# Kernel tuning notes

Hardware: AMD Instinct MI355X
Metric: run time of the kernel (lower is better)

The kernel has to match this reference:

```python
import jax, jax.numpy as jnp
import numpy as np

B, T, INPUT_DIM = 4, 2048, 1024
N_HEADS, HEAD_DIM, EMB_DIM = 16, 64, 1024


def setup_inputs() -> dict:
    key = jax.random.key(0)
    ks = jax.random.split(key, 7)
    s = 0.02
    return {
        "k": jax.random.normal(ks[0], (B, T, INPUT_DIM), jnp.float32),
        "q": jax.random.normal(ks[1], (B, T, INPUT_DIM), jnp.float32),
        "v": jax.random.normal(ks[2], (B, T, INPUT_DIM), jnp.float32),
        # weights stored [in, out] (torch Linear applies x @ W.T with W [out,in])
        "w_key": jax.random.normal(ks[3], (INPUT_DIM, N_HEADS * HEAD_DIM), jnp.float32) * s,
        "w_query": jax.random.normal(ks[4], (INPUT_DIM, N_HEADS * HEAD_DIM), jnp.float32) * s,
        "w_value": jax.random.normal(ks[5], (INPUT_DIM, N_HEADS * HEAD_DIM), jnp.float32) * s,
        "w_proj": jax.random.normal(ks[6], (N_HEADS * HEAD_DIM, EMB_DIM), jnp.float32) * s,
    }


def reference(k, q, v, w_key, w_query, w_value, w_proj):
    temperature = np.sqrt(HEAD_DIM).astype(np.float32)
    # projections -> [B, T, H, D]
    kh = (k @ w_key).reshape(B, T, N_HEADS, HEAD_DIM)
    qh = (q @ w_query).reshape(B, T, N_HEADS, HEAD_DIM)
    vh = (v @ w_value).reshape(B, T, N_HEADS, HEAD_DIM)
    # scaled dot-product attention: scores [B, H, T, T]
    scores = jnp.einsum("bqhd,bkhd->bhqk", qh, kh) / temperature
    attn = jax.nn.softmax(scores, axis=-1)
    out = jnp.einsum("bhqk,bkhd->bqhd", attn, vh).reshape(B, T, N_HEADS * HEAD_DIM)
    return out @ w_proj
```

## Files before the change

### kernel.cpp

```cpp
#include <hip/hip_runtime.h>

typedef unsigned short bf16_t;
typedef __attribute__((ext_vector_type(8))) short short8;
typedef __attribute__((ext_vector_type(4))) float f32x4;
typedef __attribute__((ext_vector_type(16))) float f32x16;
typedef __attribute__((ext_vector_type(4))) unsigned short usx4;

#define T_SEQ 2048
#define NHEAD 16

__device__ __forceinline__ unsigned short f2bf(float x) {
  union { float f; unsigned u; } v; v.f = x;
  unsigned r = v.u + 0x7fffu + ((v.u >> 16) & 1u);
  return (unsigned short)(r >> 16);
}

__device__ __forceinline__ void gld_lds16(const void* g, void* l) {
  __builtin_amdgcn_global_load_lds((const __attribute__((address_space(1))) void*)g,
                                   (__attribute__((address_space(3))) void*)l, 16, 0, 0);
}

__global__ __launch_bounds__(256) void cvt_bf16(const float* __restrict__ in,
                                                bf16_t* __restrict__ out, int n4) {
  int i = blockIdx.x * 256 + threadIdx.x;
  const int stride = gridDim.x * 256;
  for (; i < n4; i += stride) {
    const float4 v = ((const float4*)in)[i];
    usx4 w = { f2bf(v.x), f2bf(v.y), f2bf(v.z), f2bf(v.w) };
    ((usx4*)out)[i] = w;
  }
}

__global__ __launch_bounds__(256) void wtrans(const float* __restrict__ w0, const float* __restrict__ w1,
                                              const float* __restrict__ w2, const float* __restrict__ w3,
                                              bf16_t* __restrict__ wt) {
  __shared__ float tile[32][33];
  const float* w = (blockIdx.z == 0) ? w0 : (blockIdx.z == 1) ? w1 : (blockIdx.z == 2) ? w2 : w3;
  bf16_t* o = wt + (size_t)blockIdx.z * 1024 * 1024;
  const int c = threadIdx.x & 31;
  const int r = threadIdx.x >> 5;
  const int k0 = blockIdx.y * 32, n0 = blockIdx.x * 32;
#pragma unroll
  for (int rr = 0; rr < 32; rr += 8)
    tile[r + rr][c] = w[(size_t)(k0 + r + rr) * 1024 + n0 + c];
  __syncthreads();
#pragma unroll
  for (int rr = 0; rr < 32; rr += 8)
    o[(size_t)(n0 + r + rr) * 1024 + k0 + c] = f2bf(tile[c][r + rr]);
}

template<int MODE>
__global__ __launch_bounds__(256) void gemm128(const bf16_t* __restrict__ A,
                                               const bf16_t* __restrict__ Bt,
                                               void* __restrict__ Cout, int K) {
  __shared__ bf16_t As[128 * 64];
  __shared__ bf16_t Bs[128 * 64];
  const int tid = threadIdx.x;
  const int lane = tid & 63;
  const int l15 = lane & 15;
  const int g = lane >> 4;
  const int wave = tid >> 6;
  const int wr = wave >> 1, wc = wave & 1;
  const int row0 = blockIdx.y * 128, col0 = blockIdx.x * 128;

  f32x4 acc[4][4];
#pragma unroll
  for (int m = 0; m < 4; ++m)
#pragma unroll
    for (int n = 0; n < 4; ++n) acc[m][n] = (f32x4){0.f, 0.f, 0.f, 0.f};

  const int r_st = tid >> 3;
  const int c_st = tid & 7;

  for (int kt = 0; kt < K; kt += 64) {
#pragma unroll
    for (int i = 0; i < 4; ++i) {
      const int r = r_st + i * 32;
      gld_lds16(A  + (size_t)(row0 + r) * K + kt + c_st * 8, As + (size_t)(tid + i * 256) * 8);
      gld_lds16(Bt + (size_t)(col0 + r) * K + kt + c_st * 8, Bs + (size_t)(tid + i * 256) * 8);
    }
    __syncthreads();
#pragma unroll
    for (int ks = 0; ks < 2; ++ks) {
      short8 a[4], b[4];
#pragma unroll
      for (int m = 0; m < 4; ++m)
        a[m] = *(const short8*)(As + (wr * 64 + m * 16 + l15) * 64 + ks * 32 + g * 8);
#pragma unroll
      for (int n = 0; n < 4; ++n)
        b[n] = *(const short8*)(Bs + (wc * 64 + n * 16 + l15) * 64 + ks * 32 + g * 8);
#pragma unroll
      for (int m = 0; m < 4; ++m)
#pragma unroll
        for (int n = 0; n < 4; ++n)
          acc[m][n] = __builtin_amdgcn_mfma_f32_16x16x32_bf16(a[m], b[n], acc[m][n], 0, 0, 0);
    }
    __syncthreads();
  }

  if constexpr (MODE == 0 || MODE == 1) {
    const float sc = (MODE == 1) ? 0.18033688011112042f : 1.0f;
    bf16_t* C = (bf16_t*)Cout;
#pragma unroll
    for (int m = 0; m < 4; ++m) {
      const int row = row0 + wr * 64 + m * 16 + g * 4;
#pragma unroll
      for (int n = 0; n < 4; ++n) {
        const int col = col0 + wc * 64 + n * 16 + l15;
#pragma unroll
        for (int i = 0; i < 4; ++i)
          C[(size_t)(row + i) * 1024 + col] = f2bf(acc[m][n][i] * sc);
      }
    }
  } else if constexpr (MODE == 2) {
    bf16_t* C = (bf16_t*)Cout;
#pragma unroll
    for (int m = 0; m < 4; ++m) {
      const int row = row0 + wr * 64 + m * 16 + g * 4;
      const int bb = row >> 11;
      const int t = row & 2047;
#pragma unroll
      for (int n = 0; n < 4; ++n) {
        const int col = col0 + wc * 64 + n * 16 + l15;
        const int hh = col >> 6, dd = col & 63;
        usx4 w = { f2bf(acc[m][n][0]), f2bf(acc[m][n][1]), f2bf(acc[m][n][2]), f2bf(acc[m][n][3]) };
        *(usx4*)(C + (((size_t)(bb * 16 + hh) * 64 + dd) * 2048 + t)) = w;
      }
    }
  } else {
    float* C = (float*)Cout;
#pragma unroll
    for (int m = 0; m < 4; ++m) {
      const int row = row0 + wr * 64 + m * 16 + g * 4;
#pragma unroll
      for (int n = 0; n < 4; ++n) {
        const int col = col0 + wc * 64 + n * 16 + l15;
#pragma unroll
        for (int i = 0; i < 4; ++i)
          C[(size_t)(row + i) * 1024 + col] = acc[m][n][i];
      }
    }
  }
}

__global__ __launch_bounds__(256) void attn_fwd(const bf16_t* __restrict__ qh,
                                                const bf16_t* __restrict__ kh,
                                                const bf16_t* __restrict__ vt,
                                                bf16_t* __restrict__ ao) {
  __shared__ bf16_t smem[8192];
  bf16_t* Ks = smem;
  bf16_t* Vs = smem + 4096;
  const int tid = threadIdx.x;
  const int lane = tid & 63;
  const int l31 = lane & 31;
  const int half = lane >> 5;
  const int wave = tid >> 6;
  const int qblk = blockIdx.x;
  const int bh = blockIdx.y;
  const int b = bh >> 4, h = bh & 15;

  const int tq = qblk * 128 + wave * 32 + l31;
  const size_t qoff = (size_t)(b * T_SEQ + tq) * 1024 + h * 64;
  short8 qf[4];
#pragma unroll
  for (int ks = 0; ks < 4; ++ks)
    qf[ks] = *(const short8*)(qh + qoff + ks * 16 + half * 8);

  f32x16 ov0, ov1;
#pragma unroll
  for (int i = 0; i < 16; ++i) { ov0[i] = 0.f; ov1[i] = 0.f; }
  float mrun = -1e30f, lrun = 0.f;

  const size_t kbase = (size_t)b * T_SEQ * 1024 + h * 64;
  const size_t vbase = (size_t)bh * 64 * T_SEQ;
  const int r_st = tid >> 3;
  const int cd = tid & 7;

  for (int kv = 0; kv < T_SEQ / 64; ++kv) {
    const int t0 = kv * 64;
#pragma unroll
    for (int i = 0; i < 2; ++i) {
      const int r = r_st + i * 32;
      const int cs = cd ^ (r & 7);
      gld_lds16(kh + kbase + (size_t)(t0 + r) * 1024 + cs * 8, Ks + (size_t)(tid + i * 256) * 8);
      gld_lds16(vt + vbase + (size_t)r * T_SEQ + t0 + cs * 8,  Vs + (size_t)(tid + i * 256) * 8);
    }
    __syncthreads();

    f32x16 st[2];
    __builtin_amdgcn_s_setprio(1);
#pragma unroll
    for (int t = 0; t < 2; ++t) {
#pragma unroll
      for (int i = 0; i < 16; ++i) st[t][i] = 0.f;
      const int row = t * 32 + l31;
#pragma unroll
      for (int ks = 0; ks < 4; ++ks) {
        const short8 af = *(const short8*)(Ks + row * 64 + (((ks * 2 + half) ^ (l31 & 7)) * 8));
        st[t] = __builtin_amdgcn_mfma_f32_32x32x16_bf16(af, qf[ks], st[t], 0, 0, 0);
      }
    }
    __builtin_amdgcn_s_setprio(0);

    float pm = st[0][0];
#pragma unroll
    for (int i = 1; i < 16; ++i) pm = fmaxf(pm, st[0][i]);
#pragma unroll
    for (int i = 0; i < 16; ++i) pm = fmaxf(pm, st[1][i]);
    pm = fmaxf(pm, __shfl_xor(pm, 32));

    if (__any(pm > mrun + 8.f)) {
      const float newm = fmaxf(mrun, pm);
      const float corr = __builtin_amdgcn_exp2f(mrun - newm);
      mrun = newm;
      lrun *= corr;
#pragma unroll
      for (int i = 0; i < 16; ++i) { ov0[i] *= corr; ov1[i] *= corr; }
    }

    float psum = 0.f;
#pragma unroll
    for (int t = 0; t < 2; ++t)
#pragma unroll
      for (int i = 0; i < 16; ++i) {
        const float p = __builtin_amdgcn_exp2f(st[t][i] - mrun);
        st[t][i] = p;
        psum += p;
      }
    psum += __shfl_xor(psum, 32);
    lrun += psum;

#pragma unroll
    for (int s = 0; s < 4; ++s) {
      const int t = s >> 1, base = (s & 1) * 8;
      unsigned c0, c1, c2, c3;
      asm("v_cvt_pk_bf16_f32 %0, %1, %2" : "=v"(c0) : "v"(st[t][base + 0]), "v"(st[t][base + 1]));
      asm("v_cvt_pk_bf16_f32 %0, %1, %2" : "=v"(c1) : "v"(st[t][base + 2]), "v"(st[t][base + 3]));
      asm("v_cvt_pk_bf16_f32 %0, %1, %2" : "=v"(c2) : "v"(st[t][base + 4]), "v"(st[t][base + 5]));
      asm("v_cvt_pk_bf16_f32 %0, %1, %2" : "=v"(c3) : "v"(st[t][base + 6]), "v"(st[t][base + 7]));
      asm("v_permlane32_swap_b32 %0, %1" : "+v"(c0), "+v"(c2));
      asm("v_permlane32_swap_b32 %0, %1" : "+v"(c1), "+v"(c3));
      union { short8 v; unsigned u[4]; } bu;
      bu.u[0] = c0; bu.u[1] = c1; bu.u[2] = c2; bu.u[3] = c3;
      __builtin_amdgcn_s_setprio(1);
#pragma unroll
      for (int dt = 0; dt < 2; ++dt) {
        const int row = dt * 32 + l31;
        const short8 av = *(const short8*)(Vs + row * 64 + (((s * 2 + half) ^ (l31 & 7)) * 8));
        if (dt == 0) ov0 = __builtin_amdgcn_mfma_f32_32x32x16_bf16(av, bu.v, ov0, 0, 0, 0);
        else         ov1 = __builtin_amdgcn_mfma_f32_32x32x16_bf16(av, bu.v, ov1, 0, 0, 0);
      }
      __builtin_amdgcn_s_setprio(0);
    }
    __syncthreads();
  }

  const float inv = 1.f / lrun;
  bf16_t* obuf = smem + wave * 2048;
#pragma unroll
  for (int k = 0; k < 4; ++k) {
    usx4 w0 = { f2bf(ov0[4 * k + 0] * inv), f2bf(ov0[4 * k + 1] * inv),
                f2bf(ov0[4 * k + 2] * inv), f2bf(ov0[4 * k + 3] * inv) };
    *(usx4*)(obuf + l31 * 64 + ((k ^ (l31 & 7)) * 8) + half * 4) = w0;
    usx4 w1 = { f2bf(ov1[4 * k + 0] * inv), f2bf(ov1[4 * k + 1] * inv),
                f2bf(ov1[4 * k + 2] * inv), f2bf(ov1[4 * k + 3] * inv) };
    *(usx4*)(obuf + l31 * 64 + (((4 + k) ^ (l31 & 7)) * 8) + half * 4) = w1;
  }
  __syncthreads();
  const int r = lane >> 1;
  const int cb = (lane & 1) * 4;
  const size_t orow = (size_t)(b * T_SEQ + qblk * 128 + wave * 32 + r) * 1024 + h * 64;
#pragma unroll
  for (int c = 0; c < 4; ++c) {
    const int ch = cb + c;
    const short8 v = *(const short8*)(obuf + r * 64 + ((ch ^ (r & 7)) * 8));
    *(short8*)(ao + orow + ch * 8) = v;
  }
}

extern "C" void kernel_launch(void* const* d_in, const int* in_sizes, int n_in,
                              void* d_out, int out_size, void* d_ws, size_t ws_size,
                              hipStream_t stream) {
  const float* k_in  = (const float*)d_in[0];
  const float* q_in  = (const float*)d_in[1];
  const float* v_in  = (const float*)d_in[2];
  const float* w_key = (const float*)d_in[3];
  const float* w_qry = (const float*)d_in[4];
  const float* w_val = (const float*)d_in[5];
  const float* w_prj = (const float*)d_in[6];

  char* ws = (char*)d_ws;
  bf16_t* xb = (bf16_t*)(ws);
  bf16_t* wt = (bf16_t*)(ws + (16u << 20));
  bf16_t* qh = (bf16_t*)(ws + (24u << 20));
  bf16_t* kh = (bf16_t*)(ws + (40u << 20));
  bf16_t* vt = (bf16_t*)(ws + (56u << 20));
  bf16_t* ao = (bf16_t*)(ws + (72u << 20));

  wtrans<<<dim3(32, 32, 4), 256, 0, stream>>>(w_key, w_qry, w_val, w_prj, wt);

  const int N4 = (8192 * 1024) / 4;
  cvt_bf16<<<2048, 256, 0, stream>>>(k_in, xb, N4);
  gemm128<0><<<dim3(8, 64), 256, 0, stream>>>(xb, wt + 0 * (1u << 20), kh, 1024);
  cvt_bf16<<<2048, 256, 0, stream>>>(q_in, xb, N4);
  gemm128<1><<<dim3(8, 64), 256, 0, stream>>>(xb, wt + 1 * (1u << 20), qh, 1024);
  cvt_bf16<<<2048, 256, 0, stream>>>(v_in, xb, N4);
  gemm128<2><<<dim3(8, 64), 256, 0, stream>>>(xb, wt + 2 * (1u << 20), vt, 1024);

  attn_fwd<<<dim3(16, 64), 256, 0, stream>>>(qh, kh, vt, ao);

  gemm128<3><<<dim3(8, 64), 256, 0, stream>>>(ao, wt + 3 * (1u << 20), d_out, 1024);
}
```

Before: 252.4 us.

## Fuse fp32-to-bf16 conversion into GEMM loads and double-buffer attention K/V tiles

Removes the three standalone cvt_bf16 passes by having the QKV projection GEMMs read fp32 activations directly and pack them to bf16 in registers before storing to LDS. The attention kernel now double-buffers its K/V tiles so the next tile's loads overlap the current tile's compute. It also folds the running max into the score accumulator init and splits the max and sum reductions into two chains. MFMA blocks in the GEMM get raised wave priority; the register-path A load loses the async global-to-LDS path and may stall the GEMM, and attention LDS use doubles.

```diff
diff --git a/kernel.cpp b/kernel.cpp
--- a/kernel.cpp
+++ b/kernel.cpp
@@ -20,15 +20,10 @@
                                    (__attribute__((address_space(3))) void*)l, 16, 0, 0);
 }
 
-__global__ __launch_bounds__(256) void cvt_bf16(const float* __restrict__ in,
-                                                bf16_t* __restrict__ out, int n4) {
-  int i = blockIdx.x * 256 + threadIdx.x;
-  const int stride = gridDim.x * 256;
-  for (; i < n4; i += stride) {
-    const float4 v = ((const float4*)in)[i];
-    usx4 w = { f2bf(v.x), f2bf(v.y), f2bf(v.z), f2bf(v.w) };
-    ((usx4*)out)[i] = w;
-  }
+__device__ __forceinline__ unsigned cvtpk(float lo, float hi) {
+  unsigned r;
+  asm("v_cvt_pk_bf16_f32 %0, %1, %2" : "=v"(r) : "v"(lo), "v"(hi));
+  return r;
 }
 
 __global__ __launch_bounds__(256) void wtrans(const float* __restrict__ w0, const float* __restrict__ w1,
@@ -49,8 +44,8 @@
     o[(size_t)(n0 + r + rr) * 1024 + k0 + c] = f2bf(tile[c][r + rr]);
 }
 
-template<int MODE>
-__global__ __launch_bounds__(256) void gemm128(const bf16_t* __restrict__ A,
+template<int MODE, bool AFP32>
+__global__ __launch_bounds__(256) void gemm128(const void* __restrict__ A,
                                                const bf16_t* __restrict__ Bt,
                                                void* __restrict__ Cout, int K) {
   __shared__ bf16_t As[128 * 64];
@@ -76,7 +71,20 @@
 #pragma unroll
     for (int i = 0; i < 4; ++i) {
       const int r = r_st + i * 32;
-      gld_lds16(A  + (size_t)(row0 + r) * K + kt + c_st * 8, As + (size_t)(tid + i * 256) * 8);
+      if constexpr (AFP32) {
+        const float* Af = (const float*)A;
+        const float4 f0 = *(const float4*)(Af + (size_t)(row0 + r) * K + kt + c_st * 8);
+        const float4 f1 = *(const float4*)(Af + (size_t)(row0 + r) * K + kt + c_st * 8 + 4);
+        union { short8 v; unsigned u[4]; } pk;
+        pk.u[0] = cvtpk(f0.x, f0.y);
+        pk.u[1] = cvtpk(f0.z, f0.w);
+        pk.u[2] = cvtpk(f1.x, f1.y);
+        pk.u[3] = cvtpk(f1.z, f1.w);
+        *(short8*)(As + (size_t)(tid + i * 256) * 8) = pk.v;
+      } else {
+        const bf16_t* Ab = (const bf16_t*)A;
+        gld_lds16(Ab + (size_t)(row0 + r) * K + kt + c_st * 8, As + (size_t)(tid + i * 256) * 8);
+      }
       gld_lds16(Bt + (size_t)(col0 + r) * K + kt + c_st * 8, Bs + (size_t)(tid + i * 256) * 8);
     }
     __syncthreads();
@@ -89,11 +97,13 @@
 #pragma unroll
       for (int n = 0; n < 4; ++n)
         b[n] = *(const short8*)(Bs + (wc * 64 + n * 16 + l15) * 64 + ks * 32 + g * 8);
+      __builtin_amdgcn_s_setprio(1);
 #pragma unroll
       for (int m = 0; m < 4; ++m)
 #pragma unroll
         for (int n = 0; n < 4; ++n)
           acc[m][n] = __builtin_amdgcn_mfma_f32_16x16x32_bf16(a[m], b[n], acc[m][n], 0, 0, 0);
+      __builtin_amdgcn_s_setprio(0);
     }
     __syncthreads();
   }
@@ -147,9 +157,7 @@
                                                 const bf16_t* __restrict__ kh,
                                                 const bf16_t* __restrict__ vt,
                                                 bf16_t* __restrict__ ao) {
-  __shared__ bf16_t smem[8192];
-  bf16_t* Ks = smem;
-  bf16_t* Vs = smem + 4096;
+  __shared__ bf16_t smem[16384];
   const int tid = threadIdx.x;
   const int lane = tid & 63;
   const int l31 = lane & 31;
@@ -169,15 +177,17 @@
   f32x16 ov0, ov1;
 #pragma unroll
   for (int i = 0; i < 16; ++i) { ov0[i] = 0.f; ov1[i] = 0.f; }
-  float mrun = -1e30f, lrun = 0.f;
+  float mrun = 0.f, lrun = 0.f;
 
   const size_t kbase = (size_t)b * T_SEQ * 1024 + h * 64;
   const size_t vbase = (size_t)bh * 64 * T_SEQ;
   const int r_st = tid >> 3;
   const int cd = tid & 7;
 
-  for (int kv = 0; kv < T_SEQ / 64; ++kv) {
-    const int t0 = kv * 64;
+  auto stage = [&](int kvt, int bufi) {
+    bf16_t* Ks = smem + bufi * 8192;
+    bf16_t* Vs = Ks + 4096;
+    const int t0 = kvt * 64;
 #pragma unroll
     for (int i = 0; i < 2; ++i) {
       const int r = r_st + i * 32;
@@ -185,14 +195,26 @@
       gld_lds16(kh + kbase + (size_t)(t0 + r) * 1024 + cs * 8, Ks + (size_t)(tid + i * 256) * 8);
       gld_lds16(vt + vbase + (size_t)r * T_SEQ + t0 + cs * 8,  Vs + (size_t)(tid + i * 256) * 8);
     }
-    __syncthreads();
+  };
+
+  stage(0, 0);
+  __syncthreads();
+
+  for (int kv = 0; kv < T_SEQ / 64; ++kv) {
+    const int cur = kv & 1;
+    if (kv + 1 < T_SEQ / 64) stage(kv + 1, cur ^ 1);
+    const bf16_t* Ks = smem + cur * 8192;
+    const bf16_t* Vs = Ks + 4096;
 
     f32x16 st[2];
+    const float negm = -mrun;
+#pragma unroll
+    for (int t = 0; t < 2; ++t)
+#pragma unroll
+      for (int i = 0; i < 16; ++i) st[t][i] = negm;
     __builtin_amdgcn_s_setprio(1);
 #pragma unroll
     for (int t = 0; t < 2; ++t) {
-#pragma unroll
-      for (int i = 0; i < 16; ++i) st[t][i] = 0.f;
       const int row = t * 32 + l31;
 #pragma unroll
       for (int ks = 0; ks < 4; ++ks) {
@@ -202,42 +224,55 @@
     }
     __builtin_amdgcn_s_setprio(0);
 
-    float pm = st[0][0];
-#pragma unroll
-    for (int i = 1; i < 16; ++i) pm = fmaxf(pm, st[0][i]);
-#pragma unroll
-    for (int i = 0; i < 16; ++i) pm = fmaxf(pm, st[1][i]);
+    float pa = fmaxf(st[0][0], st[0][1]);
+    float pb = fmaxf(st[0][2], st[0][3]);
+#pragma unroll
+    for (int i = 4; i < 16; i += 4) {
+      pa = fmaxf(fmaxf(pa, st[0][i]), st[0][i + 1]);
+      pb = fmaxf(fmaxf(pb, st[0][i + 2]), st[0][i + 3]);
+    }
+#pragma unroll
+    for (int i = 0; i < 16; i += 4) {
+      pa = fmaxf(fmaxf(pa, st[1][i]), st[1][i + 1]);
+      pb = fmaxf(fmaxf(pb, st[1][i + 2]), st[1][i + 3]);
+    }
+    float pm = fmaxf(pa, pb);
     pm = fmaxf(pm, __shfl_xor(pm, 32));
 
-    if (__any(pm > mrun + 8.f)) {
-      const float newm = fmaxf(mrun, pm);
-      const float corr = __builtin_amdgcn_exp2f(mrun - newm);
-      mrun = newm;
+    if (__any(pm > 8.f)) {
+      const float delta = fmaxf(pm, 0.f);
+      mrun += delta;
+      const float corr = __builtin_amdgcn_exp2f(-delta);
       lrun *= corr;
 #pragma unroll
       for (int i = 0; i < 16; ++i) { ov0[i] *= corr; ov1[i] *= corr; }
-    }
-
-    float psum = 0.f;
+#pragma unroll
+      for (int t = 0; t < 2; ++t)
+#pragma unroll
+        for (int i = 0; i < 16; ++i) st[t][i] -= delta;
+    }
+
+    float ps0 = 0.f, ps1 = 0.f;
 #pragma unroll
     for (int t = 0; t < 2; ++t)
 #pragma unroll
-      for (int i = 0; i < 16; ++i) {
-        const float p = __builtin_amdgcn_exp2f(st[t][i] - mrun);
-        st[t][i] = p;
-        psum += p;
-      }
+      for (int i = 0; i < 16; i += 2) {
+        const float p0 = __builtin_amdgcn_exp2f(st[t][i]);
+        const float p1 = __builtin_amdgcn_exp2f(st[t][i + 1]);
+        st[t][i] = p0; st[t][i + 1] = p1;
+        ps0 += p0; ps1 += p1;
+      }
+    float psum = ps0 + ps1;
     psum += __shfl_xor(psum, 32);
     lrun += psum;
 
 #pragma unroll
     for (int s = 0; s < 4; ++s) {
       const int t = s >> 1, base = (s & 1) * 8;
-      unsigned c0, c1, c2, c3;
-      asm("v_cvt_pk_bf16_f32 %0, %1, %2" : "=v"(c0) : "v"(st[t][base + 0]), "v"(st[t][base + 1]));
-      asm("v_cvt_pk_bf16_f32 %0, %1, %2" : "=v"(c1) : "v"(st[t][base + 2]), "v"(st[t][base + 3]));
-      asm("v_cvt_pk_bf16_f32 %0, %1, %2" : "=v"(c2) : "v"(st[t][base + 4]), "v"(st[t][base + 5]));
-      asm("v_cvt_pk_bf16_f32 %0, %1, %2" : "=v"(c3) : "v"(st[t][base + 6]), "v"(st[t][base + 7]));
+      unsigned c0 = cvtpk(st[t][base + 0], st[t][base + 1]);
+      unsigned c1 = cvtpk(st[t][base + 2], st[t][base + 3]);
+      unsigned c2 = cvtpk(st[t][base + 4], st[t][base + 5]);
+      unsigned c3 = cvtpk(st[t][base + 6], st[t][base + 7]);
       asm("v_permlane32_swap_b32 %0, %1" : "+v"(c0), "+v"(c2));
       asm("v_permlane32_swap_b32 %0, %1" : "+v"(c1), "+v"(c3));
       union { short8 v; unsigned u[4]; } bu;
@@ -290,24 +325,19 @@
   const float* w_prj = (const float*)d_in[6];
 
   char* ws = (char*)d_ws;
-  bf16_t* xb = (bf16_t*)(ws);
-  bf16_t* wt = (bf16_t*)(ws + (16u << 20));
-  bf16_t* qh = (bf16_t*)(ws + (24u << 20));
-  bf16_t* kh = (bf16_t*)(ws + (40u << 20));
-  bf16_t* vt = (bf16_t*)(ws + (56u << 20));
-  bf16_t* ao = (bf16_t*)(ws + (72u << 20));
+  bf16_t* wt = (bf16_t*)(ws);
+  bf16_t* qh = (bf16_t*)(ws + ( 8u << 20));
+  bf16_t* kh = (bf16_t*)(ws + (24u << 20));
+  bf16_t* vt = (bf16_t*)(ws + (40u << 20));
+  bf16_t* ao = (bf16_t*)(ws + (56u << 20));
 
   wtrans<<<dim3(32, 32, 4), 256, 0, stream>>>(w_key, w_qry, w_val, w_prj, wt);
 
-  const int N4 = (8192 * 1024) / 4;
-  cvt_bf16<<<2048, 256, 0, stream>>>(k_in, xb, N4);
-  gemm128<0><<<dim3(8, 64), 256, 0, stream>>>(xb, wt + 0 * (1u << 20), kh, 1024);
-  cvt_bf16<<<2048, 256, 0, stream>>>(q_in, xb, N4);
-  gemm128<1><<<dim3(8, 64), 256, 0, stream>>>(xb, wt + 1 * (1u << 20), qh, 1024);
-  cvt_bf16<<<2048, 256, 0, stream>>>(v_in, xb, N4);
-  gemm128<2><<<dim3(8, 64), 256, 0, stream>>>(xb, wt + 2 * (1u << 20), vt, 1024);
+  gemm128<0, true><<<dim3(8, 64), 256, 0, stream>>>(k_in, wt + 0 * (1u << 20), kh, 1024);
+  gemm128<1, true><<<dim3(8, 64), 256, 0, stream>>>(q_in, wt + 1 * (1u << 20), qh, 1024);
+  gemm128<2, true><<<dim3(8, 64), 256, 0, stream>>>(v_in, wt + 2 * (1u << 20), vt, 1024);
 
   attn_fwd<<<dim3(16, 64), 256, 0, stream>>>(qh, kh, vt, ao);
 
-  gemm128<3><<<dim3(8, 64), 256, 0, stream>>>(ao, wt + 3 * (1u << 20), d_out, 1024);
-}
+  gemm128<3, false><<<dim3(8, 64), 256, 0, stream>>>(ao, wt + 3 * (1u << 20), d_out, 1024);
+}
```

Result: slower. 265.4 us (+5.2%).
